# Kernel optimization log

Hardware: AMD Instinct MI355X
Metric: run time of the kernel (lower is better)

Reference implementation:

```python
import jax, jax.numpy as jnp
import numpy as np

N_NODES = 100000
N_EDGES = 1600000
D_IN, D_HID, D_OUT = 128, 64, 40


def glorot(key, shape):
    lim = float(np.sqrt(6.0 / (shape[0] + shape[1])))
    return jax.random.uniform(key, shape, jnp.float32, -lim, lim)


def gcn_layer(x, W, b, src, dst, d_inv):
    # PyG GCNConv: linear first, then sym-normalized aggregation with self-loops.
    h = x @ W  # [N, d_out]
    coef = (d_inv[src] * d_inv[dst])[:, None]       # [E, 1]
    msg = h[src] * coef                              # [E, d_out] gather
    agg = jax.ops.segment_sum(msg, dst, num_segments=N_NODES)  # scatter-add
    agg = agg + h * (d_inv * d_inv)[:, None]         # self-loop contribution
    return agg + b


def setup_inputs() -> dict:
    key = jax.random.key(0)
    ks = jax.random.split(key, 8)
    x = jax.random.normal(ks[0], (N_NODES, D_IN), jnp.float32)
    edge_index = jax.random.randint(ks[1], (2, N_EDGES), 0, N_NODES, jnp.int64)
    return {
        "x": x,
        "edge_index": edge_index,
        "W1": glorot(ks[2], (D_IN, D_HID)), "b1": jnp.zeros((D_HID,), jnp.float32),
        "W2": glorot(ks[3], (D_HID, D_HID)), "b2": jnp.zeros((D_HID,), jnp.float32),
        "W3": glorot(ks[4], (D_HID, D_OUT)), "b3": jnp.zeros((D_OUT,), jnp.float32),
    }


def reference(x, edge_index, W1, b1, W2, b2, W3, b3):
    src, dst = edge_index[0], edge_index[1]
    # degree with self-loops (each node gets +1)
    deg = jax.ops.segment_sum(jnp.ones((N_EDGES,), jnp.float32), dst,
                              num_segments=N_NODES) + 1.0
    d_inv = jax.lax.rsqrt(deg)
    h = jax.nn.relu(gcn_layer(x, W1, b1, src, dst, d_inv))
    h = jax.nn.relu(gcn_layer(h, W2, b2, src, dst, d_inv))
    return gcn_layer(h, W3, b3, src, dst, d_inv)
```

## Files before the change

### kernel.cpp

```cpp
#include <hip/hip_runtime.h>
#include <hip/hip_bf16.h>


constexpr int BLK = 256;
constexpr int SB2 = 9;
constexpr int EPB = 4096;

__device__ inline unsigned short bf_rne(float f) {
    unsigned int u = __float_as_uint(f);
    unsigned int r = (u + 0x7fffu + ((u >> 16) & 1u)) >> 16;
    return (unsigned short)r;
}
__device__ inline unsigned int pk(unsigned short lo, unsigned short hi) {
    return (unsigned int)lo | ((unsigned int)hi << 16);
}

__global__ __launch_bounds__(256) void part_hist(
    const int* __restrict__ dst, int* __restrict__ bh, int E, int nblk, int NB2) {
    __shared__ int lh[256];
    int k = blockIdx.x, t = threadIdx.x;
    lh[t] = 0;
    __syncthreads();
    int e0 = k * EPB;
#pragma unroll
    for (int j = 0; j < EPB / 256; ++j) {
        int e = e0 + j * 256 + t;
        if (e < E) atomicAdd(&lh[dst[e] >> SB2], 1);
    }
    __syncthreads();
    if (t < NB2) bh[t * nblk + k] = lh[t];
}

__global__ __launch_bounds__(256) void bucket_totals(
    const int* __restrict__ bh, int* __restrict__ btot, int nblk) {
    __shared__ int sh[256];
    int b = blockIdx.x, t = threadIdx.x;
    int s = 0;
    for (int i = t; i < nblk; i += 256) s += bh[b * nblk + i];
    sh[t] = s;
    __syncthreads();
    for (int off = 128; off > 0; off >>= 1) {
        if (t < off) sh[t] += sh[t + off];
        __syncthreads();
    }
    if (t == 0) btot[b] = sh[0];
}

__global__ void bucket_scan(const int* __restrict__ btot, int* __restrict__ bbase, int NB2) {
    __shared__ int sh[256];
    int t = threadIdx.x;
    int v = (t < NB2) ? btot[t] : 0;
    sh[t] = v;
    __syncthreads();
    for (int off = 1; off < 256; off <<= 1) {
        int x = (t >= off) ? sh[t - off] : 0;
        __syncthreads();
        sh[t] += x;
        __syncthreads();
    }
    if (t < NB2) bbase[t] = sh[t] - v;
}

__global__ __launch_bounds__(256) void part_scan(
    int* __restrict__ bh, const int* __restrict__ bbase, int nblk) {
    __shared__ int sh[256];
    int b = blockIdx.x, t = threadIdx.x;
    int base = bbase[b];
    int v[4]; int s = 0;
#pragma unroll
    for (int j = 0; j < 4; ++j) {
        int idx = t * 4 + j;
        v[j] = (idx < nblk) ? bh[b * nblk + idx] : 0;
        s += v[j];
    }
    sh[t] = s;
    __syncthreads();
    for (int off = 1; off < 256; off <<= 1) {
        int x = (t >= off) ? sh[t - off] : 0;
        __syncthreads();
        sh[t] += x;
        __syncthreads();
    }
    int run = sh[t] - s;
#pragma unroll
    for (int j = 0; j < 4; ++j) {
        int idx = t * 4 + j;
        if (idx < nblk) bh[b * nblk + idx] = base + run;
        run += v[j];
    }
}

__global__ __launch_bounds__(256) void part_scatter(
    const int* __restrict__ src, const int* __restrict__ dst,
    const int* __restrict__ bh, unsigned int* __restrict__ buf,
    int E, int nblk, int NB2) {
    __shared__ int lbase[256];
    __shared__ int lcnt[256];
    int k = blockIdx.x, t = threadIdx.x;
    lcnt[t] = 0;
    if (t < NB2) lbase[t] = bh[t * nblk + k];
    __syncthreads();
    int e0 = k * EPB;
#pragma unroll
    for (int j = 0; j < EPB / 256; ++j) {
        int e = e0 + j * 256 + t;
        if (e < E) {
            int d = dst[e];
            int b = d >> SB2;
            int p = lbase[b] + atomicAdd(&lcnt[b], 1);
            buf[p] = ((unsigned int)(d & ((1 << SB2) - 1)) << 23) | (unsigned int)src[e];
        }
    }
}

__global__ __launch_bounds__(256) void csr_finalize(
    const unsigned int* __restrict__ buf, const int* __restrict__ bbase,
    int* __restrict__ row_ptr, float* __restrict__ dinv,
    int* __restrict__ csr, int N, int E, int NB2) {
    __shared__ int hist[1 << SB2];
    __shared__ int excl[1 << SB2];
    __shared__ int ssc[256];
    int b = blockIdx.x, t = threadIdx.x;
    int nb0 = b << SB2;
    int nn = N - nb0; if (nn > (1 << SB2)) nn = 1 << SB2;
    int beg = bbase[b];
    int end = (b + 1 < NB2) ? bbase[b + 1] : E;

    hist[t] = 0; hist[t + 256] = 0;
    __syncthreads();
    for (int i = beg + t; i < end; i += 256)
        atomicAdd(&hist[buf[i] >> 23], 1);
    __syncthreads();

    int a0 = hist[2 * t], a1 = hist[2 * t + 1];
    int s = a0 + a1;
    ssc[t] = s;
    __syncthreads();
    for (int off = 1; off < 256; off <<= 1) {
        int x = (t >= off) ? ssc[t - off] : 0;
        __syncthreads();
        ssc[t] += x;
        __syncthreads();
    }
    int run = ssc[t] - s;
    excl[2 * t] = run;
    excl[2 * t + 1] = run + a0;
    __syncthreads();

    for (int j = t; j < nn; j += 256) {
        row_ptr[nb0 + j] = beg + excl[j];
        dinv[nb0 + j] = rsqrtf((float)hist[j] + 1.0f);
    }
    if (b == NB2 - 1 && t == 0) row_ptr[N] = E;
    __syncthreads();

    hist[t] = 0; hist[t + 256] = 0;
    __syncthreads();
    for (int i = beg + t; i < end; i += 256) {
        unsigned int w = buf[i];
        int local = w >> 23;
        int p = beg + excl[local] + atomicAdd(&hist[local], 1);
        csr[p] = (int)(w & 0x7fffffu);
    }
}

template<int K, int NOUT>
__global__ __launch_bounds__(256) void gemm_scale(
    const float* __restrict__ X, const float* __restrict__ W,
    const float* __restrict__ d_inv, unsigned short* __restrict__ hs, int M)
{
    __shared__ float Wl[K * 64];
    __shared__ float Xt[16][68];

    int t = threadIdx.x;
    for (int idx = t; idx < K * 64; idx += 256) {
        int k = idx >> 6, c = idx & 63;
        Wl[idx] = (c < NOUT) ? W[k * NOUT + c] : 0.0f;
    }

    int row0 = blockIdx.x * 64;
    int tr = t >> 4, tc = t & 15;
    int lr = t >> 2, lq = t & 3;
    float a[4][4] = {};

    for (int k0 = 0; k0 < K; k0 += 16) {
        __syncthreads();
        int grow = row0 + lr;
        float4 xv = make_float4(0.f, 0.f, 0.f, 0.f);
        if (grow < M) xv = *(const float4*)(X + (size_t)grow * K + k0 + lq * 4);
        Xt[lq * 4 + 0][lr] = xv.x; Xt[lq * 4 + 1][lr] = xv.y;
        Xt[lq * 4 + 2][lr] = xv.z; Xt[lq * 4 + 3][lr] = xv.w;
        __syncthreads();

#pragma unroll 4
        for (int kk = 0; kk < 16; ++kk) {
            float4 xr = *(const float4*)(&Xt[kk][tr * 4]);
            float4 wr = *(const float4*)(&Wl[(k0 + kk) * 64 + tc * 4]);
            const float xs[4] = {xr.x, xr.y, xr.z, xr.w};
            const float wsr[4] = {wr.x, wr.y, wr.z, wr.w};
#pragma unroll
            for (int i = 0; i < 4; ++i)
#pragma unroll
                for (int j = 0; j < 4; ++j)
                    a[i][j] += xs[i] * wsr[j];
        }
    }

#pragma unroll
    for (int i = 0; i < 4; ++i) {
        int r = row0 + tr * 4 + i;
        if (r < M) {
            float s = d_inv[r];
            int c = tc * 4;
            float v0 = (c + 0 < NOUT) ? a[i][0] * s : 0.0f;
            float v1 = (c + 1 < NOUT) ? a[i][1] * s : 0.0f;
            float v2 = (c + 2 < NOUT) ? a[i][2] * s : 0.0f;
            float v3 = (c + 3 < NOUT) ? a[i][3] * s : 0.0f;
            uint2 u;
            u.x = pk(bf_rne(v0), bf_rne(v1));
            u.y = pk(bf_rne(v2), bf_rne(v3));
            *(uint2*)(hs + (size_t)r * 64 + c) = u;
        }
    }
}

template<int DACT, bool RELU, int OSTRIDE>
__global__ __launch_bounds__(256) void agg8(
    const unsigned short* __restrict__ hs, const int* __restrict__ row_ptr,
    const int* __restrict__ csr, const float* __restrict__ dinv,
    const float* __restrict__ b, float* __restrict__ out, int N)
{
    int wave = (blockIdx.x * 256 + threadIdx.x) >> 6;
    int lane = threadIdx.x & 63;
    if (wave >= N) return;
    int i = wave;
    int g = lane >> 3, q = lane & 7;
    const uint4* hsv = (const uint4*)hs;

    int beg = row_ptr[i], end = row_ptr[i + 1];
    float acc[8] = {0.f, 0.f, 0.f, 0.f, 0.f, 0.f, 0.f, 0.f};

    for (int c = beg; c < end; c += 64) {
        int m = end - c; if (m > 64) m = 64;
        int s_l = (c + lane < end) ? csr[c + lane] : 0;
        int nIter = (m + 7) >> 3;
        for (int k = 0; k < nIter; ++k) {
            int ei = k * 8 + g;
            int s = __shfl(s_l, ei, 64);
            if (ei < m) {
                uint4 u = hsv[(size_t)s * 8 + q];
                acc[0] += __uint_as_float(u.x << 16);
                acc[1] += __uint_as_float(u.x & 0xffff0000u);
                acc[2] += __uint_as_float(u.y << 16);
                acc[3] += __uint_as_float(u.y & 0xffff0000u);
                acc[4] += __uint_as_float(u.z << 16);
                acc[5] += __uint_as_float(u.z & 0xffff0000u);
                acc[6] += __uint_as_float(u.w << 16);
                acc[7] += __uint_as_float(u.w & 0xffff0000u);
            }
        }
    }

#pragma unroll
    for (int off = 8; off < 64; off <<= 1)
#pragma unroll
        for (int j = 0; j < 8; ++j)
            acc[j] += __shfl_xor(acc[j], off, 64);

    if (g == 0 && q * 8 < DACT) {
        uint4 u = hsv[(size_t)i * 8 + q];
        acc[0] += __uint_as_float(u.x << 16);
        acc[1] += __uint_as_float(u.x & 0xffff0000u);
        acc[2] += __uint_as_float(u.y << 16);
        acc[3] += __uint_as_float(u.y & 0xffff0000u);
        acc[4] += __uint_as_float(u.z << 16);
        acc[5] += __uint_as_float(u.z & 0xffff0000u);
        acc[6] += __uint_as_float(u.w << 16);
        acc[7] += __uint_as_float(u.w & 0xffff0000u);
        float di = dinv[i];
        const float4 b0 = *(const float4*)(b + q * 8);
        const float4 b1 = *(const float4*)(b + q * 8 + 4);
        float4 v0, v1;
        v0.x = di * acc[0] + b0.x; v0.y = di * acc[1] + b0.y;
        v0.z = di * acc[2] + b0.z; v0.w = di * acc[3] + b0.w;
        v1.x = di * acc[4] + b1.x; v1.y = di * acc[5] + b1.y;
        v1.z = di * acc[6] + b1.z; v1.w = di * acc[7] + b1.w;
        if (RELU) {
            v0.x = fmaxf(v0.x, 0.f); v0.y = fmaxf(v0.y, 0.f);
            v0.z = fmaxf(v0.z, 0.f); v0.w = fmaxf(v0.w, 0.f);
            v1.x = fmaxf(v1.x, 0.f); v1.y = fmaxf(v1.y, 0.f);
            v1.z = fmaxf(v1.z, 0.f); v1.w = fmaxf(v1.w, 0.f);
        }
        *(float4*)(out + (size_t)i * OSTRIDE + q * 8)     = v0;
        *(float4*)(out + (size_t)i * OSTRIDE + q * 8 + 4) = v1;
    }
}

extern "C" void kernel_launch(void* const* d_in, const int* in_sizes, int n_in,
                              void* d_out, int out_size, void* d_ws, size_t ws_size,
                              hipStream_t stream) {
    const float* x   = (const float*)d_in[0];
    const int*   ei  = (const int*)  d_in[1];
    const float* W1  = (const float*)d_in[2];
    const float* bb1 = (const float*)d_in[3];
    const float* W2  = (const float*)d_in[4];
    const float* bb2 = (const float*)d_in[5];
    const float* W3  = (const float*)d_in[6];
    const float* bb3 = (const float*)d_in[7];
    float* out = (float*)d_out;

    const int N = in_sizes[0] / 128;
    const int E = in_sizes[1] / 2;
    const int* src = ei;
    const int* dst = ei + E;
    const int NB2  = (N + (1 << SB2) - 1) >> SB2;
    const int nblk = (E + EPB - 1) / EPB;

    float* ws = (float*)d_ws;
    const size_t NP  = ((size_t)N + 255) & ~255ull;
    const size_t N64 = (size_t)N * 64;
    float* dinv = ws;
    unsigned short* bufHs = (unsigned short*)(ws + NP);
    float* bufO = ws + NP + (size_t)N * 32;
    int*   row_ptr = (int*)(bufO + N64);
    int*   btot    = row_ptr + (((size_t)N + 2) & ~1ull);
    int*   bbase   = btot + 256;
    int*   bh      = bbase + 256;
    size_t bhsz    = ((size_t)NB2 * nblk + 1) & ~1ull;
    unsigned int* buf = (unsigned int*)(bh + bhsz);
    int*   csr     = (int*)(buf + E);

    dim3 blk(BLK);
    int gRows = (N + 63) / 64;
    int gWave = (N * 64 + BLK - 1) / BLK;

    part_hist<<<nblk, blk, 0, stream>>>(dst, bh, E, nblk, NB2);
    bucket_totals<<<NB2, blk, 0, stream>>>(bh, btot, nblk);
    bucket_scan<<<1, blk, 0, stream>>>(btot, bbase, NB2);
    part_scan<<<NB2, blk, 0, stream>>>(bh, bbase, nblk);
    part_scatter<<<nblk, blk, 0, stream>>>(src, dst, bh, buf, E, nblk, NB2);
    csr_finalize<<<NB2, blk, 0, stream>>>(buf, bbase, row_ptr, dinv, csr, N, E, NB2);

    gemm_scale<128, 64><<<gRows, blk, 0, stream>>>(x, W1, dinv, bufHs, N);
    agg8<64, true, 64><<<gWave, blk, 0, stream>>>(bufHs, row_ptr, csr, dinv, bb1, bufO, N);

    gemm_scale<64, 64><<<gRows, blk, 0, stream>>>(bufO, W2, dinv, bufHs, N);
    agg8<64, true, 64><<<gWave, blk, 0, stream>>>(bufHs, row_ptr, csr, dinv, bb2, bufO, N);

    gemm_scale<64, 40><<<gRows, blk, 0, stream>>>(bufO, W3, dinv, bufHs, N);
    agg8<40, false, 40><<<gWave, blk, 0, stream>>>(bufHs, row_ptr, csr, dinv, bb3, out, N);
}
```

Measured before the change: 353.4 us.

## Use bf16 MFMA for dense transforms and store hidden activations as bf16

Replaces the FP32 SIMT tiled GEMM with a kernel built on the 16x16x32 bf16 MFMA instruction. Weights are converted to bf16 in LDS, and results are staged through LDS before scaling and packing. The intermediate aggregation outputs are now written as bf16 instead of fp32, which halves activation traffic between layers and lets the next GEMM load bf16 fragments directly. The trade is lower precision, since both inputs and weights are rounded to bf16, and the GEMMs are a modest share of runtime next to the gather aggregation.

```diff
diff --git a/kernel.cpp b/kernel.cpp
--- a/kernel.cpp
+++ b/kernel.cpp
@@ -5,6 +5,9 @@
 constexpr int BLK = 256;
 constexpr int SB2 = 9;
 constexpr int EPB = 4096;
+
+typedef __attribute__((ext_vector_type(8))) short bf16x8;
+typedef __attribute__((ext_vector_type(4))) float f32x4;
 
 __device__ inline unsigned short bf_rne(float f) {
     unsigned int u = __float_as_uint(f);
@@ -164,71 +167,86 @@
     }
 }
 
-template<int K, int NOUT>
-__global__ __launch_bounds__(256) void gemm_scale(
-    const float* __restrict__ X, const float* __restrict__ W,
+template<int K, int NOUT, bool AFP32>
+__global__ __launch_bounds__(256) void gemm_mfma(
+    const void* __restrict__ Aptr, const float* __restrict__ W,
     const float* __restrict__ d_inv, unsigned short* __restrict__ hs, int M)
 {
-    __shared__ float Wl[K * 64];
-    __shared__ float Xt[16][68];
-
-    int t = threadIdx.x;
+    __shared__ unsigned short Wt[64][K + 8];
+    __shared__ float Cst[64][68];
+
+    const int t = threadIdx.x;
+    const int wave = t >> 6, lane = t & 63;
+    const int m = lane & 15, kq = lane >> 4;
+
     for (int idx = t; idx < K * 64; idx += 256) {
         int k = idx >> 6, c = idx & 63;
-        Wl[idx] = (c < NOUT) ? W[k * NOUT + c] : 0.0f;
-    }
-
-    int row0 = blockIdx.x * 64;
-    int tr = t >> 4, tc = t & 15;
-    int lr = t >> 2, lq = t & 3;
-    float a[4][4] = {};
-
-    for (int k0 = 0; k0 < K; k0 += 16) {
-        __syncthreads();
-        int grow = row0 + lr;
-        float4 xv = make_float4(0.f, 0.f, 0.f, 0.f);
-        if (grow < M) xv = *(const float4*)(X + (size_t)grow * K + k0 + lq * 4);
-        Xt[lq * 4 + 0][lr] = xv.x; Xt[lq * 4 + 1][lr] = xv.y;
-        Xt[lq * 4 + 2][lr] = xv.z; Xt[lq * 4 + 3][lr] = xv.w;
-        __syncthreads();
-
-#pragma unroll 4
-        for (int kk = 0; kk < 16; ++kk) {
-            float4 xr = *(const float4*)(&Xt[kk][tr * 4]);
-            float4 wr = *(const float4*)(&Wl[(k0 + kk) * 64 + tc * 4]);
-            const float xs[4] = {xr.x, xr.y, xr.z, xr.w};
-            const float wsr[4] = {wr.x, wr.y, wr.z, wr.w};
-#pragma unroll
-            for (int i = 0; i < 4; ++i)
-#pragma unroll
-                for (int j = 0; j < 4; ++j)
-                    a[i][j] += xs[i] * wsr[j];
-        }
-    }
-
-#pragma unroll
-    for (int i = 0; i < 4; ++i) {
-        int r = row0 + tr * 4 + i;
-        if (r < M) {
-            float s = d_inv[r];
-            int c = tc * 4;
-            float v0 = (c + 0 < NOUT) ? a[i][0] * s : 0.0f;
-            float v1 = (c + 1 < NOUT) ? a[i][1] * s : 0.0f;
-            float v2 = (c + 2 < NOUT) ? a[i][2] * s : 0.0f;
-            float v3 = (c + 3 < NOUT) ? a[i][3] * s : 0.0f;
-            uint2 u;
-            u.x = pk(bf_rne(v0), bf_rne(v1));
-            u.y = pk(bf_rne(v2), bf_rne(v3));
-            *(uint2*)(hs + (size_t)r * 64 + c) = u;
-        }
-    }
-}
-
-template<int DACT, bool RELU, int OSTRIDE>
+        float wv = (c < NOUT) ? W[k * NOUT + c] : 0.0f;
+        Wt[c][k] = bf_rne(wv);
+    }
+    __syncthreads();
+
+    const int rb = blockIdx.x * 64;
+    int arow = rb + wave * 16 + m;
+    if (arow >= M) arow = M - 1;
+
+    f32x4 acc[4] = {{0.f,0.f,0.f,0.f},{0.f,0.f,0.f,0.f},
+                    {0.f,0.f,0.f,0.f},{0.f,0.f,0.f,0.f}};
+    union Frag { bf16x8 v; unsigned short u[8]; };
+
+#pragma unroll
+    for (int kc = 0; kc < K / 32; ++kc) {
+        const int kbase = kc * 32 + kq * 8;
+        Frag a;
+        if (AFP32) {
+            const float* ap = (const float*)Aptr + (size_t)arow * K + kbase;
+            float4 x0 = *(const float4*)ap;
+            float4 x1 = *(const float4*)(ap + 4);
+            a.u[0] = bf_rne(x0.x); a.u[1] = bf_rne(x0.y);
+            a.u[2] = bf_rne(x0.z); a.u[3] = bf_rne(x0.w);
+            a.u[4] = bf_rne(x1.x); a.u[5] = bf_rne(x1.y);
+            a.u[6] = bf_rne(x1.z); a.u[7] = bf_rne(x1.w);
+        } else {
+            const unsigned short* ap = (const unsigned short*)Aptr + (size_t)arow * 64 + kbase;
+            a.v = *(const bf16x8*)ap;
+        }
+#pragma unroll
+        for (int ct = 0; ct < 4; ++ct) {
+            Frag b;
+            b.v = *(const bf16x8*)(&Wt[ct * 16 + m][kbase]);
+            acc[ct] = __builtin_amdgcn_mfma_f32_16x16x32_bf16(a.v, b.v, acc[ct], 0, 0, 0);
+        }
+    }
+
+#pragma unroll
+    for (int ct = 0; ct < 4; ++ct)
+#pragma unroll
+        for (int r = 0; r < 4; ++r)
+            Cst[wave * 16 + kq * 4 + r][ct * 16 + m] = acc[ct][r];
+    __syncthreads();
+
+    int row = t >> 2, seg = t & 3;
+    int grow = rb + row;
+    if (grow < M) {
+        float di = d_inv[grow];
+        unsigned int uu[8];
+#pragma unroll
+        for (int j = 0; j < 8; ++j) {
+            float v0 = Cst[row][seg * 16 + 2 * j]     * di;
+            float v1 = Cst[row][seg * 16 + 2 * j + 1] * di;
+            uu[j] = pk(bf_rne(v0), bf_rne(v1));
+        }
+        unsigned short* orow = hs + (size_t)grow * 64 + seg * 16;
+        *(uint4*)orow       = make_uint4(uu[0], uu[1], uu[2], uu[3]);
+        *((uint4*)orow + 1) = make_uint4(uu[4], uu[5], uu[6], uu[7]);
+    }
+}
+
+template<int DACT, bool RELU, bool OBF16, int OSTRIDE>
 __global__ __launch_bounds__(256) void agg8(
     const unsigned short* __restrict__ hs, const int* __restrict__ row_ptr,
     const int* __restrict__ csr, const float* __restrict__ dinv,
-    const float* __restrict__ b, float* __restrict__ out, int N)
+    const float* __restrict__ b, void* __restrict__ out, int N)
 {
     int wave = (blockIdx.x * 256 + threadIdx.x) >> 6;
     int lane = threadIdx.x & 63;
@@ -278,21 +296,26 @@
         acc[6] += __uint_as_float(u.w << 16);
         acc[7] += __uint_as_float(u.w & 0xffff0000u);
         float di = dinv[i];
-        const float4 b0 = *(const float4*)(b + q * 8);
-        const float4 b1 = *(const float4*)(b + q * 8 + 4);
-        float4 v0, v1;
-        v0.x = di * acc[0] + b0.x; v0.y = di * acc[1] + b0.y;
-        v0.z = di * acc[2] + b0.z; v0.w = di * acc[3] + b0.w;
-        v1.x = di * acc[4] + b1.x; v1.y = di * acc[5] + b1.y;
-        v1.z = di * acc[6] + b1.z; v1.w = di * acc[7] + b1.w;
-        if (RELU) {
-            v0.x = fmaxf(v0.x, 0.f); v0.y = fmaxf(v0.y, 0.f);
-            v0.z = fmaxf(v0.z, 0.f); v0.w = fmaxf(v0.w, 0.f);
-            v1.x = fmaxf(v1.x, 0.f); v1.y = fmaxf(v1.y, 0.f);
-            v1.z = fmaxf(v1.z, 0.f); v1.w = fmaxf(v1.w, 0.f);
-        }
-        *(float4*)(out + (size_t)i * OSTRIDE + q * 8)     = v0;
-        *(float4*)(out + (size_t)i * OSTRIDE + q * 8 + 4) = v1;
+#pragma unroll
+        for (int j = 0; j < 8; ++j) {
+            acc[j] = di * acc[j] + b[q * 8 + j];
+            if (RELU) acc[j] = fmaxf(acc[j], 0.0f);
+        }
+        if (OBF16) {
+            unsigned short* ob = (unsigned short*)out;
+            uint4 o;
+            o.x = pk(bf_rne(acc[0]), bf_rne(acc[1]));
+            o.y = pk(bf_rne(acc[2]), bf_rne(acc[3]));
+            o.z = pk(bf_rne(acc[4]), bf_rne(acc[5]));
+            o.w = pk(bf_rne(acc[6]), bf_rne(acc[7]));
+            *(uint4*)(ob + (size_t)i * 64 + q * 8) = o;
+        } else {
+            float* of = (float*)out;
+            *(float4*)(of + (size_t)i * OSTRIDE + q * 8) =
+                make_float4(acc[0], acc[1], acc[2], acc[3]);
+            *(float4*)(of + (size_t)i * OSTRIDE + q * 8 + 4) =
+                make_float4(acc[4], acc[5], acc[6], acc[7]);
+        }
     }
 }
 
@@ -318,11 +341,10 @@
 
     float* ws = (float*)d_ws;
     const size_t NP  = ((size_t)N + 255) & ~255ull;
-    const size_t N64 = (size_t)N * 64;
     float* dinv = ws;
-    unsigned short* bufHs = (unsigned short*)(ws + NP);
-    float* bufO = ws + NP + (size_t)N * 32;
-    int*   row_ptr = (int*)(bufO + N64);
+    unsigned short* bufHs  = (unsigned short*)(ws + NP);
+    unsigned short* bufAct = bufHs + (size_t)N * 64;
+    int*   row_ptr = (int*)(bufAct + (size_t)N * 64);
     int*   btot    = row_ptr + (((size_t)N + 2) & ~1ull);
     int*   bbase   = btot + 256;
     int*   bh      = bbase + 256;
@@ -341,12 +363,12 @@
     part_scatter<<<nblk, blk, 0, stream>>>(src, dst, bh, buf, E, nblk, NB2);
     csr_finalize<<<NB2, blk, 0, stream>>>(buf, bbase, row_ptr, dinv, csr, N, E, NB2);
 
-    gemm_scale<128, 64><<<gRows, blk, 0, stream>>>(x, W1, dinv, bufHs, N);
-    agg8<64, true, 64><<<gWave, blk, 0, stream>>>(bufHs, row_ptr, csr, dinv, bb1, bufO, N);
-
-    gemm_scale<64, 64><<<gRows, blk, 0, stream>>>(bufO, W2, dinv, bufHs, N);
-    agg8<64, true, 64><<<gWave, blk, 0, stream>>>(bufHs, row_ptr, csr, dinv, bb2, bufO, N);
-
-    gemm_scale<64, 40><<<gRows, blk, 0, stream>>>(bufO, W3, dinv, bufHs, N);
-    agg8<40, false, 40><<<gWave, blk, 0, stream>>>(bufHs, row_ptr, csr, dinv, bb3, out, N);
-}
+    gemm_mfma<128, 64, true><<<gRows, blk, 0, stream>>>(x, W1, dinv, bufHs, N);
+    agg8<64, true, true, 64><<<gWave, blk, 0, stream>>>(bufHs, row_ptr, csr, dinv, bb1, bufAct, N);
+
+    gemm_mfma<64, 64, false><<<gRows, blk, 0, stream>>>(bufAct, W2, dinv, bufHs, N);
+    agg8<64, true, true, 64><<<gWave, blk, 0, stream>>>(bufHs, row_ptr, csr, dinv, bb2, bufAct, N);
+
+    gemm_mfma<64, 40, false><<<gRows, blk, 0, stream>>>(bufAct, W3, dinv, bufHs, N);
+    agg8<40, false, false, 40><<<gWave, blk, 0, stream>>>(bufHs, row_ptr, csr, dinv, bb3, out, N);
+}
```

Result: faster. 325.9 us (-7.8%).
